# Optimization experiments

Measured on AMD Instinct MI355X. Metric: run time of the kernel, lower is better.

The kernel has to match this reference:

```python
import jax, jax.numpy as jnp
from jax import lax
import numpy as np

B, L, D, F, T, NB = 32, 512, 256, 256, 2048, 256
LN_EPS = 1e-5


def _layer_norm(h, g, b):
    m = jnp.mean(h, axis=-1, keepdims=True)
    v = jnp.mean((h - m) ** 2, axis=-1, keepdims=True)
    return (h - m) * lax.rsqrt(v + LN_EPS) * g + b


def _predictor(h, prm):
    # Conv1d(k=3, pad=1) -> ReLU -> LayerNorm, twice, then Linear(F->1) -> ReLU -> squeeze
    # (dropout is identity in this deterministic reference)
    c1w, c1b, g1, b1, c2w, c2b, g2, b2, lw, lb = prm
    h = lax.conv_general_dilated(h, c1w, (1,), 'SAME', dimension_numbers=('NWC', 'WIO', 'NWC')) + c1b
    h = _layer_norm(jax.nn.relu(h), g1, b1)
    h = lax.conv_general_dilated(h, c2w, (1,), 'SAME', dimension_numbers=('NWC', 'WIO', 'NWC')) + c2b
    h = _layer_norm(jax.nn.relu(h), g2, b2)
    return jax.nn.relu(jnp.einsum('btf,f->bt', h, lw) + lb)  # [B, T]


def _length_regulate(x, dur, t_out):
    # Gather-based equivalent of the dense alignment-matrix matmul in LengthRegulator.LR:
    # frame t maps to phoneme j with cum[j-1] <= t < cum[j]; frames past total duration are zero.
    cum = jnp.cumsum(dur, axis=1)                                          # [B, L]
    t = jnp.arange(t_out)                                                  # [T]
    idx = jax.vmap(lambda c: jnp.searchsorted(c, t, side='right'))(cum)    # [B, T]
    valid = idx < dur.shape[1]
    idx = jnp.clip(idx, 0, dur.shape[1] - 1)
    out = jnp.take_along_axis(x, idx[..., None], axis=1)                   # [B, T, D]
    return jnp.where(valid[..., None], out, jnp.zeros((), x.dtype))


def setup_inputs() -> dict:
    key = jax.random.key(0)
    ks = iter(jax.random.split(key, 64))

    def nrm(shape, s=0.05):
        return jax.random.normal(next(ks), shape, jnp.float32) * s

    inp = dict(
        x=jax.random.normal(next(ks), (B, L, D), jnp.float32),
        d_target=jax.random.randint(next(ks), (B, L), 0, 4, jnp.int32),
        e_target=jax.random.normal(next(ks), (B, T), jnp.float32),
        p_target=jax.random.normal(next(ks), (B, T), jnp.float32),
        mel_max_length=T,
    )
    for p in ('dur', 'en', 'pi'):
        inp[p + '_c1w'] = nrm((3, D, F)); inp[p + '_c1b'] = jnp.zeros((F,), jnp.float32)
        inp[p + '_g1'] = jnp.ones((F,), jnp.float32); inp[p + '_b1'] = jnp.zeros((F,), jnp.float32)
        inp[p + '_c2w'] = nrm((3, F, F)); inp[p + '_c2b'] = jnp.zeros((F,), jnp.float32)
        inp[p + '_g2'] = jnp.ones((F,), jnp.float32); inp[p + '_b2'] = jnp.zeros((F,), jnp.float32)
        inp[p + '_lw'] = nrm((F,)); inp[p + '_lb'] = jnp.zeros((), jnp.float32)
    inp['en_emb'] = nrm((NB, D), 0.1)
    inp['pi_emb'] = nrm((NB, D), 0.1)
    inp['en_bins'] = jnp.linspace(-3.0, 3.0, NB - 1, dtype=jnp.float32)
    inp['pi_bins'] = jnp.linspace(-3.0, 3.0, NB - 1, dtype=jnp.float32)
    return inp


def reference(x, d_target, e_target, p_target, mel_max_length,
              dur_c1w, dur_c1b, dur_g1, dur_b1, dur_c2w, dur_c2b, dur_g2, dur_b2, dur_lw, dur_lb,
              en_c1w, en_c1b, en_g1, en_b1, en_c2w, en_c2b, en_g2, en_b2, en_lw, en_lb,
              pi_c1w, pi_c1b, pi_g1, pi_b1, pi_c2w, pi_c2b, pi_g2, pi_b2, pi_lw, pi_lb,
              en_emb, pi_emb, en_bins, pi_bins):
    dur_prm = (dur_c1w, dur_c1b, dur_g1, dur_b1, dur_c2w, dur_c2b, dur_g2, dur_b2, dur_lw, dur_lb)
    en_prm = (en_c1w, en_c1b, en_g1, en_b1, en_c2w, en_c2b, en_g2, en_b2, en_lw, en_lb)
    pi_prm = (pi_c1w, pi_c1b, pi_g1, pi_b1, pi_c2w, pi_c2b, pi_g2, pi_b2, pi_lw, pi_lb)

    log_dur = _predictor(x, dur_prm)                               # [B, L]
    h = _length_regulate(x, d_target, mel_max_length)              # [B, T, D]

    energy_pred = _predictor(h, en_prm)                            # [B, T]
    e_idx = jnp.searchsorted(en_bins, e_target, side='left')       # torch.bucketize(right=False)
    h = h + jnp.take(en_emb, e_idx, axis=0)

    pitch_pred = _predictor(h, pi_prm)                             # [B, T]
    p_idx = jnp.searchsorted(pi_bins, p_target, side='left')
    h = h + jnp.take(pi_emb, p_idx, axis=0)

    return (h, log_dur, pitch_pred, energy_pred)
```

## Files before the change

kernel.cpp:

```cpp
#include <hip/hip_runtime.h>
#include <hip/hip_bf16.h>
#include <cstddef>

constexpr int B = 32, L = 512, D = 256, F = 256, T = 2048, NB = 256;
constexpr float LN_EPS = 1e-5f;
constexpr int BDIM = 256;
constexpr int WFRAGS = 24 * 16 * 64;

constexpr int N_FH  = 1024;
constexpr int NT_L  = 9;
constexpr int NT_T  = 34;
constexpr int N_DUR = NT_L * B;
constexpr int N_TP  = NT_T * B;

typedef __attribute__((ext_vector_type(8))) short short8;
typedef __attribute__((ext_vector_type(4))) short short4v;
typedef __attribute__((ext_vector_type(4))) float f32x4;

__device__ inline short f2bf(float x) {
    __hip_bfloat16 h = __float2bfloat16(x);
    return __builtin_bit_cast(short, h);
}

__global__ void cumsum_kernel(const int* __restrict__ dt, int* __restrict__ cum) {
    __shared__ int s[L];
    const int b = blockIdx.x, tid = threadIdx.x;
    s[tid] = dt[b * L + tid];
    __syncthreads();
    for (int off = 1; off < L; off <<= 1) {
        int v = (tid >= off) ? s[tid - off] : 0;
        __syncthreads();
        s[tid] += v;
        __syncthreads();
    }
    cum[b * L + tid] = s[tid];
}

__global__ void idx_kernel(const int* __restrict__ cum,
                           const float* __restrict__ et, const float* __restrict__ ebins,
                           const float* __restrict__ pt, const float* __restrict__ pbins,
                           int* __restrict__ gidx, int* __restrict__ eidx, int* __restrict__ pidx) {
    const int r = blockIdx.x * BDIM + threadIdx.x;
    const int b = r >> 11, t = r & (T - 1);
    const int* c = cum + b * L;
    int lo = 0, hi = L;
    while (lo < hi) { const int mid = (lo + hi) >> 1; if (c[mid] <= t) lo = mid + 1; else hi = mid; }
    gidx[r] = (lo < L) ? lo : -1;
    const float e = et[r];
    int el = 0, eh = NB - 1;
    while (el < eh) { const int mid = (el + eh) >> 1; if (ebins[mid] < e) el = mid + 1; else eh = mid; }
    eidx[r] = el;
    const float p = pt[r];
    int pl = 0, ph = NB - 1;
    while (pl < ph) { const int mid = (pl + ph) >> 1; if (pbins[mid] < p) pl = mid + 1; else ph = mid; }
    pidx[r] = pl;
}

__global__ void wprep_kernel(const float* __restrict__ w0, const float* __restrict__ w1,
                             const float* __restrict__ w2, const float* __restrict__ w3,
                             const float* __restrict__ w4, const float* __restrict__ w5,
                             short* __restrict__ wb) {
    const float* ws[6] = {w0, w1, w2, w3, w4, w5};
    const float* w = ws[blockIdx.y];
    short* dst = wb + (size_t)blockIdx.y * WFRAGS * 8;
    const int phi = blockIdx.x * BDIM + threadIdx.x;
    const int kb = phi >> 10;
    const int n16 = (phi >> 6) & 15;
    const int lane = phi & 63;
    const int kconv = kb >> 3, dblk = kb & 7;
    const int kg = lane >> 4;
    const int fcol = (n16 >> 2) * 64 + (lane & 15) * 4 + (n16 & 3);
    const float* src = w + (size_t)kconv * D * F + (dblk * 32 + kg * 8) * F + fcol;
    short8 o;
    #pragma unroll
    for (int j = 0; j < 8; j++) o[j] = f2bf(src[j * F]);
    *(short8*)(dst + (size_t)phi * 8) = o;
}

__global__ void zv_kernel(const float* __restrict__ cb1, const float* __restrict__ g1,
                          const float* __restrict__ b1,
                          const float* __restrict__ w2, const float* __restrict__ cb2,
                          const float* __restrict__ g2, const float* __restrict__ b2,
                          const float* __restrict__ lw, const float* __restrict__ lb,
                          float* __restrict__ zv) {
    __shared__ float z1s[F];
    __shared__ float red[8];
    const int f = threadIdx.x;
    const int wv = f >> 6, lane = f & 63;

    float v = fmaxf(cb1[f], 0.f);
    float s = v, q = v * v;
    #pragma unroll
    for (int msk = 1; msk < 64; msk <<= 1) { s += __shfl_xor(s, msk); q += __shfl_xor(q, msk); }
    if (lane == 0) { red[wv] = s; red[4 + wv] = q; }
    __syncthreads();
    {
        const float S = red[0] + red[1] + red[2] + red[3];
        const float Q = red[4] + red[5] + red[6] + red[7];
        const float m = S * (1.f / 256.f);
        const float var = fmaxf(Q * (1.f / 256.f) - m * m, 0.f);
        const float rs = rsqrtf(var + LN_EPS);
        z1s[f] = (v - m) * rs * g1[f] + b1[f];
    }
    __syncthreads();

    float y = cb2[f];
    for (int d = 0; d < D; d++) {
        y += z1s[d] * (w2[(size_t)d * F + f] + w2[((size_t)D + d) * F + f]
                       + w2[((size_t)2 * D + d) * F + f]);
    }
    v = fmaxf(y, 0.f);
    s = v; q = v * v;
    #pragma unroll
    for (int msk = 1; msk < 64; msk <<= 1) { s += __shfl_xor(s, msk); q += __shfl_xor(q, msk); }
    __syncthreads();
    if (lane == 0) { red[wv] = s; red[4 + wv] = q; }
    __syncthreads();
    const float S = red[0] + red[1] + red[2] + red[3];
    const float Q = red[4] + red[5] + red[6] + red[7];
    const float m = S * (1.f / 256.f);
    const float var = fmaxf(Q * (1.f / 256.f) - m * m, 0.f);
    const float rs = rsqrtf(var + LN_EPS);
    float p = ((v - m) * rs * g2[f] + b2[f]) * lw[f];
    #pragma unroll
    for (int msk = 1; msk < 64; msk <<= 1) p += __shfl_xor(p, msk);
    __syncthreads();
    if (lane == 0) red[wv] = p;
    __syncthreads();
    if (f == 0) zv[0] = fmaxf(red[0] + red[1] + red[2] + red[3] + lb[0], 0.f);
}

__device__ __forceinline__ void conv_mfma16(const short8 (&a)[4], const short8 (&bb)[4],
                                            f32x4 (&acc)[4][4]) {
    __builtin_amdgcn_s_setprio(1);
    #pragma unroll
    for (int m = 0; m < 4; m++)
        #pragma unroll
        for (int n = 0; n < 4; n++)
            acc[m][n] = __builtin_amdgcn_mfma_f32_16x16x32_bf16(a[m], bb[n], acc[m][n], 0, 0, 0);
    __builtin_amdgcn_s_setprio(0);
}

__device__ __forceinline__ void conv_kloop(const short* in_s, const short8* bw,
                                           f32x4 (&acc)[4][4], int w,
                                           int lane, int kg, int lr) {
    const short8* bp = bw + (w * 4) * 64 + lane;
    short8 bA[4], bB[4];
    #pragma unroll
    for (int n = 0; n < 4; n++) bA[n] = bp[n * 64];
    bp += 1024;
    #pragma unroll
    for (int n = 0; n < 4; n++) bB[n] = bp[n * 64];
    bp += 1024;

    #pragma unroll
    for (int kconv = 0; kconv < 3; kconv++) {
        const short* rowp = in_s + (lr + kconv) * 256;
        const int xb = (lr + kconv) & 7;
        #pragma unroll 1
        for (int db = 0; db < 8; db += 2) {
            short8 a[4];
            {
                const short* ab = rowp + (((db * 4 + kg) ^ xb) << 3);
                #pragma unroll
                for (int m = 0; m < 4; m++) a[m] = *(const short8*)(ab + m * 4096);
                conv_mfma16(a, bA, acc);
                #pragma unroll
                for (int n = 0; n < 4; n++) bA[n] = bp[n * 64];
                bp += 1024;
            }
            {
                const short* ab = rowp + ((((db + 1) * 4 + kg) ^ xb) << 3);
                #pragma unroll
                for (int m = 0; m < 4; m++) a[m] = *(const short8*)(ab + m * 4096);
                conv_mfma16(a, bB, acc);
                #pragma unroll
                for (int n = 0; n < 4; n++) bB[n] = bp[n * 64];
                bp += 1024;
            }
        }
    }
}

struct PredParams {
    const short* wb1; const short* wb2;
    const float *cb1, *g1, *b1, *cb2, *g2, *b2, *lw, *lb;
    const int* eidx; const float* emb;
    const float* zv;
    float* out;
    int Tlen;
    int mode;
};

__launch_bounds__(BDIM, 4)
__global__ void mega_kernel(const float* __restrict__ xin,
                            const int* __restrict__ gidx,
                            const int* __restrict__ cum,
                            const int* __restrict__ eidxA,
                            const int* __restrict__ pidxA,
                            const float* __restrict__ eemb,
                            const float* __restrict__ pemb,
                            float* __restrict__ h,
                            PredParams pd, PredParams pe, PredParams pp) {
    __shared__ short in_s[66 * 256];
    __shared__ float red_s[4][64], red_q[4][64];
    __shared__ float row_m[64], row_rs[64];
    __shared__ float dot_p[4][64];

    const int tid = threadIdx.x;
    const int w = tid >> 6, lane = tid & 63;

    int id = blockIdx.x;
    if (id < N_FH) {
        const int row0 = id * 64 + w * 16;
        #pragma unroll 4
        for (int i = 0; i < 16; i++) {
            const int row = row0 + i;
            const int b = row >> 11;
            const int g = gidx[row], ei = eidxA[row], pi = pidxA[row];
            float4 v = make_float4(0.f, 0.f, 0.f, 0.f);
            if (g >= 0) v = *(const float4*)(xin + ((size_t)b * L + g) * D + lane * 4);
            const float4 ev = *(const float4*)(eemb + (size_t)ei * D + lane * 4);
            const float4 pv = *(const float4*)(pemb + (size_t)pi * D + lane * 4);
            v.x += ev.x + pv.x; v.y += ev.y + pv.y; v.z += ev.z + pv.z; v.w += ev.w + pv.w;
            *(float4*)(h + (size_t)row * D + lane * 4) = v;
        }
        return;
    }
    id -= N_FH;

    PredParams P;
    int b, tx;
    if (id < N_DUR) {
        P = pd; b = id / NT_L; tx = id % NT_L;
    } else if (id < N_DUR + N_TP) {
        id -= N_DUR;
        P = pe; b = id / NT_T; tx = id % NT_T;
    } else {
        id -= N_DUR + N_TP;
        P = pp; b = id / NT_T; tx = id % NT_T;
    }
    const int Tlen = P.Tlen;
    const int t0 = tx * 62;
    const int kg = lane >> 4, lr = lane & 15;

    if (P.zv != nullptr) {
        const int ctot = cum[(b + 1) * L - 1];
        if (t0 - 2 >= ctot) {
            if (tid < 62) {
                const int t = t0 + tid;
                if (t < Tlen) P.out[(size_t)b * Tlen + t] = P.zv[0];
            }
            return;
        }
    }

    constexpr int TASKS = 66 * 32;
    constexpr int BATCH = 4;
    const bool has_emb = (P.emb != nullptr);
    for (int base = 0; base < TASKS; base += BATCH * BDIM) {
        float4 fa[BATCH], fb[BATCH], ea[BATCH], eb[BATCH];
        #pragma unroll
        for (int j = 0; j < BATCH; j++) {
            fa[j] = make_float4(0.f, 0.f, 0.f, 0.f); fb[j] = fa[j];
            ea[j] = fa[j]; eb[j] = fa[j];
            const int task = base + j * BDIM + tid;
            if (task < TASKS) {
                const int row = task >> 5, slot = task & 31;
                const int t = t0 - 2 + row;
                if (t >= 0 && t < Tlen) {
                    if (P.mode == 0) {
                        const float* p = xin + ((size_t)b * Tlen + t) * D + slot * 8;
                        fa[j] = *(const float4*)p; fb[j] = *(const float4*)(p + 4);
                    } else {
                        const int g = gidx[b * T + t];
                        if (g >= 0) {
                            const float* p = xin + ((size_t)b * L + g) * D + slot * 8;
                            fa[j] = *(const float4*)p; fb[j] = *(const float4*)(p + 4);
                        }
                        if (has_emb) {
                            const float* er = P.emb + (size_t)P.eidx[b * T + t] * F + slot * 8;
                            ea[j] = *(const float4*)er; eb[j] = *(const float4*)(er + 4);
                        }
                    }
                }
            }
        }
        #pragma unroll
        for (int j = 0; j < BATCH; j++) {
            const int task = base + j * BDIM + tid;
            if (task < TASKS) {
                const int row = task >> 5, slot = task & 31;
                short8 frag;
                frag[0] = f2bf(fa[j].x + ea[j].x); frag[1] = f2bf(fa[j].y + ea[j].y);
                frag[2] = f2bf(fa[j].z + ea[j].z); frag[3] = f2bf(fa[j].w + ea[j].w);
                frag[4] = f2bf(fb[j].x + eb[j].x); frag[5] = f2bf(fb[j].y + eb[j].y);
                frag[6] = f2bf(fb[j].z + eb[j].z); frag[7] = f2bf(fb[j].w + eb[j].w);
                *(short8*)(in_s + row * 256 + ((slot ^ (row & 7)) << 3)) = frag;
            }
        }
    }
    __syncthreads();

    f32x4 acc[4][4];
    #pragma unroll
    for (int m = 0; m < 4; m++)
        #pragma unroll
        for (int n = 0; n < 4; n++)
            acc[m][n] = (f32x4){0.f, 0.f, 0.f, 0.f};
    conv_kloop(in_s, (const short8*)P.wb1, acc, w, lane, kg, lr);

    const int cbase = w * 64 + lr * 4;
    const f32x4 c1v = *(const f32x4*)(P.cb1 + cbase);
    const f32x4 g1v = *(const f32x4*)(P.g1 + cbase);
    const f32x4 b1v = *(const f32x4*)(P.b1 + cbase);

    #pragma unroll
    for (int m = 0; m < 4; m++) {
        #pragma unroll
        for (int reg = 0; reg < 4; reg++) {
            float s = 0.f, q = 0.f;
            #pragma unroll
            for (int n = 0; n < 4; n++) {
                const float v = fmaxf(acc[m][n][reg] + c1v[n], 0.f);
                acc[m][n][reg] = v;
                s += v; q += v * v;
            }
            #pragma unroll
            for (int msk = 1; msk < 16; msk <<= 1) { s += __shfl_xor(s, msk); q += __shfl_xor(q, msk); }
            if (lr == 0) {
                const int r = m * 16 + kg * 4 + reg;
                red_s[w][r] = s; red_q[w][r] = q;
            }
        }
    }
    __syncthreads();
    if (tid < 64) {
        const float s = red_s[0][tid] + red_s[1][tid] + red_s[2][tid] + red_s[3][tid];
        const float q = red_q[0][tid] + red_q[1][tid] + red_q[2][tid] + red_q[3][tid];
        const float mm = s * (1.f / 256.f);
        const float var = fmaxf(q * (1.f / 256.f) - mm * mm, 0.f);
        row_m[tid] = mm;
        row_rs[tid] = rsqrtf(var + LN_EPS);
    }
    if (tid >= 128 && tid < 192) {
        short8 z = {};
        *(short8*)(in_s + 64 * 256 + (tid - 128) * 8) = z;
    }
    __syncthreads();

    #pragma unroll
    for (int m = 0; m < 4; m++) {
        #pragma unroll
        for (int reg = 0; reg < 4; reg++) {
            const int r1 = m * 16 + kg * 4 + reg;
            const int tg = t0 - 1 + r1;
            const bool ok = (tg >= 0) && (tg < Tlen);
            const float mm = row_m[r1], rs = row_rs[r1];
            short4v o;
            #pragma unroll
            for (int n = 0; n < 4; n++) {
                const float v = ok ? (acc[m][n][reg] - mm) * rs * g1v[n] + b1v[n] : 0.f;
                o[n] = f2bf(v);
            }
            *(short4v*)(in_s + r1 * 256 + (((cbase >> 3) ^ (r1 & 7)) << 3) + (cbase & 7)) = o;
        }
    }
    __syncthreads();

    #pragma unroll
    for (int m = 0; m < 4; m++)
        #pragma unroll
        for (int n = 0; n < 4; n++)
            acc[m][n] = (f32x4){0.f, 0.f, 0.f, 0.f};
    conv_kloop(in_s, (const short8*)P.wb2, acc, w, lane, kg, lr);

    const f32x4 c2v = *(const f32x4*)(P.cb2 + cbase);
    const f32x4 g2v = *(const f32x4*)(P.g2 + cbase);
    const f32x4 b2v = *(const f32x4*)(P.b2 + cbase);
    const f32x4 lwv = *(const f32x4*)(P.lw + cbase);

    #pragma unroll
    for (int m = 0; m < 4; m++) {
        #pragma unroll
        for (int reg = 0; reg < 4; reg++) {
            float s = 0.f, q = 0.f;
            #pragma unroll
            for (int n = 0; n < 4; n++) {
                const float v = fmaxf(acc[m][n][reg] + c2v[n], 0.f);
                acc[m][n][reg] = v;
                s += v; q += v * v;
            }
            #pragma unroll
            for (int msk = 1; msk < 16; msk <<= 1) { s += __shfl_xor(s, msk); q += __shfl_xor(q, msk); }
            if (lr == 0) {
                const int r = m * 16 + kg * 4 + reg;
                red_s[w][r] = s; red_q[w][r] = q;
            }
        }
    }
    __syncthreads();
    if (tid < 64) {
        const float s = red_s[0][tid] + red_s[1][tid] + red_s[2][tid] + red_s[3][tid];
        const float q = red_q[0][tid] + red_q[1][tid] + red_q[2][tid] + red_q[3][tid];
        const float mm = s * (1.f / 256.f);
        const float var = fmaxf(q * (1.f / 256.f) - mm * mm, 0.f);
        row_m[tid] = mm;
        row_rs[tid] = rsqrtf(var + LN_EPS);
    }
    __syncthreads();
    #pragma unroll
    for (int m = 0; m < 4; m++) {
        #pragma unroll
        for (int reg = 0; reg < 4; reg++) {
            const int r = m * 16 + kg * 4 + reg;
            const float mm = row_m[r], rs = row_rs[r];
            float p = 0.f;
            #pragma unroll
            for (int n = 0; n < 4; n++)
                p += ((acc[m][n][reg] - mm) * rs * g2v[n] + b2v[n]) * lwv[n];
            #pragma unroll
            for (int msk = 1; msk < 16; msk <<= 1) p += __shfl_xor(p, msk);
            if (lr == 0) dot_p[w][r] = p;
        }
    }
    __syncthreads();
    if (tid < 62) {
        const int t = t0 + tid;
        if (t < Tlen) {
            const float p = dot_p[0][tid] + dot_p[1][tid] + dot_p[2][tid] + dot_p[3][tid] + P.lb[0];
            P.out[(size_t)b * Tlen + t] = fmaxf(p, 0.f);
        }
    }
}

extern "C" void kernel_launch(void* const* d_in, const int* in_sizes, int n_in,
                              void* d_out, int out_size, void* d_ws, size_t ws_size,
                              hipStream_t stream) {
    const float* x        = (const float*)d_in[0];
    const int*   d_target = (const int*)d_in[1];
    const float* e_target = (const float*)d_in[2];
    const float* p_target = (const float*)d_in[3];

    const float* const* P = (const float* const*)d_in;
    const float* en_emb  = (const float*)d_in[35];
    const float* pi_emb  = (const float*)d_in[36];
    const float* en_bins = (const float*)d_in[37];
    const float* pi_bins = (const float*)d_in[38];

    float* out = (float*)d_out;
    float* h        = out;
    float* log_dur  = out + (size_t)B * T * D;
    float* pitch    = log_dur + (size_t)B * L;
    float* energy   = pitch + (size_t)B * T;

    short* wbs  = (short*)d_ws;
    int*   cum  = (int*)(wbs + (size_t)6 * WFRAGS * 8);
    int*   gidx = cum + B * L;
    int*   eidx = gidx + B * T;
    int*   pidx = eidx + B * T;
    float* zvp  = (float*)(pidx + B * T);

    wprep_kernel<<<dim3(WFRAGS / BDIM, 6), BDIM, 0, stream>>>(
        P[5], P[9], P[15], P[19], P[25], P[29], wbs);

    cumsum_kernel<<<B, L, 0, stream>>>(d_target, cum);
    idx_kernel<<<B * T / BDIM, BDIM, 0, stream>>>(
        cum, e_target, en_bins, p_target, pi_bins, gidx, eidx, pidx);

    zv_kernel<<<1, BDIM, 0, stream>>>(
        P[16], P[17], P[18], P[19], P[20], P[21], P[22], P[23], P[24], zvp);

    PredParams dur_p = { wbs + (size_t)0 * WFRAGS * 8, wbs + (size_t)1 * WFRAGS * 8,
                         P[6], P[7], P[8], P[10], P[11], P[12], P[13], P[14],
                         nullptr, nullptr, nullptr, log_dur, L, 0 };
    PredParams en_p  = { wbs + (size_t)2 * WFRAGS * 8, wbs + (size_t)3 * WFRAGS * 8,
                         P[16], P[17], P[18], P[20], P[21], P[22], P[23], P[24],
                         nullptr, nullptr, zvp, energy, T, 1 };
    PredParams pi_p  = { wbs + (size_t)4 * WFRAGS * 8, wbs + (size_t)5 * WFRAGS * 8,
                         P[26], P[27], P[28], P[30], P[31], P[32], P[33], P[34],
                         eidx, en_emb, nullptr, pitch, T, 1 };

    mega_kernel<<<N_FH + N_DUR + 2 * N_TP, BDIM, 0, stream>>>(
        x, gidx, cum, eidx, pidx, en_emb, pi_emb, h, dur_p, en_p, pi_p);
}
```

Before: 153.1 us.

## Merge preprocessing kernels into one preamble launch and reorder mega-kernel blocks

Replaces four small launches (weight prep, cumsum, index search, zero-vector predictor) with a single preamble kernel whose blocks pick their role from the block index. The cumsum and the binary searches now share one block per batch, so the cumulative durations are read from shared memory. The mega kernel now schedules predictor blocks first and the memory-bound frame-gather blocks last, so heavy work starts earlier and the gather fills the tail. This cuts launch overhead and inter-kernel gaps, but the idx work now runs on only 32 blocks instead of 256.

```diff
diff --git a/kernel.cpp b/kernel.cpp
--- a/kernel.cpp
+++ b/kernel.cpp
@@ -12,6 +12,11 @@
 constexpr int NT_T  = 34;
 constexpr int N_DUR = NT_L * B;
 constexpr int N_TP  = NT_T * B;
+constexpr int N_PRED = N_DUR + 2 * N_TP;
+
+constexpr int PRE_WPREP = 576;
+constexpr int PRE_IDX   = 32;
+constexpr int PRE_TOTAL = PRE_WPREP + PRE_IDX + 1;
 
 typedef __attribute__((ext_vector_type(8))) short short8;
 typedef __attribute__((ext_vector_type(4))) short short4v;
@@ -22,112 +27,123 @@
     return __builtin_bit_cast(short, h);
 }
 
-__global__ void cumsum_kernel(const int* __restrict__ dt, int* __restrict__ cum) {
-    __shared__ int s[L];
-    const int b = blockIdx.x, tid = threadIdx.x;
-    s[tid] = dt[b * L + tid];
-    __syncthreads();
-    for (int off = 1; off < L; off <<= 1) {
-        int v = (tid >= off) ? s[tid - off] : 0;
-        __syncthreads();
-        s[tid] += v;
-        __syncthreads();
-    }
-    cum[b * L + tid] = s[tid];
-}
-
-__global__ void idx_kernel(const int* __restrict__ cum,
-                           const float* __restrict__ et, const float* __restrict__ ebins,
-                           const float* __restrict__ pt, const float* __restrict__ pbins,
-                           int* __restrict__ gidx, int* __restrict__ eidx, int* __restrict__ pidx) {
-    const int r = blockIdx.x * BDIM + threadIdx.x;
-    const int b = r >> 11, t = r & (T - 1);
-    const int* c = cum + b * L;
-    int lo = 0, hi = L;
-    while (lo < hi) { const int mid = (lo + hi) >> 1; if (c[mid] <= t) lo = mid + 1; else hi = mid; }
-    gidx[r] = (lo < L) ? lo : -1;
-    const float e = et[r];
-    int el = 0, eh = NB - 1;
-    while (el < eh) { const int mid = (el + eh) >> 1; if (ebins[mid] < e) el = mid + 1; else eh = mid; }
-    eidx[r] = el;
-    const float p = pt[r];
-    int pl = 0, ph = NB - 1;
-    while (pl < ph) { const int mid = (pl + ph) >> 1; if (pbins[mid] < p) pl = mid + 1; else ph = mid; }
-    pidx[r] = pl;
-}
-
-__global__ void wprep_kernel(const float* __restrict__ w0, const float* __restrict__ w1,
-                             const float* __restrict__ w2, const float* __restrict__ w3,
-                             const float* __restrict__ w4, const float* __restrict__ w5,
-                             short* __restrict__ wb) {
-    const float* ws[6] = {w0, w1, w2, w3, w4, w5};
-    const float* w = ws[blockIdx.y];
-    short* dst = wb + (size_t)blockIdx.y * WFRAGS * 8;
-    const int phi = blockIdx.x * BDIM + threadIdx.x;
-    const int kb = phi >> 10;
-    const int n16 = (phi >> 6) & 15;
-    const int lane = phi & 63;
-    const int kconv = kb >> 3, dblk = kb & 7;
-    const int kg = lane >> 4;
-    const int fcol = (n16 >> 2) * 64 + (lane & 15) * 4 + (n16 & 3);
-    const float* src = w + (size_t)kconv * D * F + (dblk * 32 + kg * 8) * F + fcol;
-    short8 o;
-    #pragma unroll
-    for (int j = 0; j < 8; j++) o[j] = f2bf(src[j * F]);
-    *(short8*)(dst + (size_t)phi * 8) = o;
-}
-
-__global__ void zv_kernel(const float* __restrict__ cb1, const float* __restrict__ g1,
-                          const float* __restrict__ b1,
-                          const float* __restrict__ w2, const float* __restrict__ cb2,
-                          const float* __restrict__ g2, const float* __restrict__ b2,
-                          const float* __restrict__ lw, const float* __restrict__ lb,
-                          float* __restrict__ zv) {
-    __shared__ float z1s[F];
+__global__ void preamble_kernel(const float* __restrict__ w0, const float* __restrict__ w1,
+                                const float* __restrict__ w2, const float* __restrict__ w3,
+                                const float* __restrict__ w4, const float* __restrict__ w5,
+                                const int* __restrict__ dt,
+                                const float* __restrict__ et, const float* __restrict__ ebins,
+                                const float* __restrict__ pt, const float* __restrict__ pbins,
+                                const float* __restrict__ zcb1, const float* __restrict__ zg1,
+                                const float* __restrict__ zb1, const float* __restrict__ zw2,
+                                const float* __restrict__ zcb2, const float* __restrict__ zg2,
+                                const float* __restrict__ zb2, const float* __restrict__ zlw,
+                                const float* __restrict__ zlb,
+                                short* __restrict__ wb, int* __restrict__ cum,
+                                int* __restrict__ gidx, int* __restrict__ eidx,
+                                int* __restrict__ pidx, float* __restrict__ zv) {
+    __shared__ int   cs[512];
+    __shared__ float z1s[256];
     __shared__ float red[8];
-    const int f = threadIdx.x;
-    const int wv = f >> 6, lane = f & 63;
-
-    float v = fmaxf(cb1[f], 0.f);
-    float s = v, q = v * v;
-    #pragma unroll
-    for (int msk = 1; msk < 64; msk <<= 1) { s += __shfl_xor(s, msk); q += __shfl_xor(q, msk); }
-    if (lane == 0) { red[wv] = s; red[4 + wv] = q; }
-    __syncthreads();
+
+    const int tid = threadIdx.x;
+    int id = blockIdx.x;
+
+    if (id < PRE_WPREP) {
+        const float* ws[6] = {w0, w1, w2, w3, w4, w5};
+        const float* w = ws[id / 96];
+        short* dst = wb + (size_t)(id / 96) * WFRAGS * 8;
+        const int phi = (id % 96) * BDIM + tid;
+        const int kb = phi >> 10;
+        const int n16 = (phi >> 6) & 15;
+        const int lane = phi & 63;
+        const int kconv = kb >> 3, dblk = kb & 7;
+        const int kg = lane >> 4;
+        const int fcol = (n16 >> 2) * 64 + (lane & 15) * 4 + (n16 & 3);
+        const float* src = w + (size_t)kconv * D * F + (dblk * 32 + kg * 8) * F + fcol;
+        short8 o;
+        #pragma unroll
+        for (int j = 0; j < 8; j++) o[j] = f2bf(src[j * F]);
+        *(short8*)(dst + (size_t)phi * 8) = o;
+        return;
+    }
+    id -= PRE_WPREP;
+
+    if (id < PRE_IDX) {
+        const int b = id;
+        cs[tid] = dt[b * L + tid];
+        cs[tid + 256] = dt[b * L + tid + 256];
+        __syncthreads();
+        for (int off = 1; off < 512; off <<= 1) {
+            const int v0 = (tid >= off) ? cs[tid - off] : 0;
+            const int v1 = (tid + 256 >= off) ? cs[tid + 256 - off] : 0;
+            __syncthreads();
+            cs[tid] += v0; cs[tid + 256] += v1;
+            __syncthreads();
+        }
+        cum[b * L + tid] = cs[tid];
+        cum[b * L + tid + 256] = cs[tid + 256];
+        #pragma unroll
+        for (int i = 0; i < 8; i++) {
+            const int t = tid + i * 256;
+            const int r = b * T + t;
+            int lo = 0, hi = L;
+            while (lo < hi) { const int mid = (lo + hi) >> 1; if (cs[mid] <= t) lo = mid + 1; else hi = mid; }
+            gidx[r] = (lo < L) ? lo : -1;
+            const float e = et[r];
+            int el = 0, eh = NB - 1;
+            while (el < eh) { const int mid = (el + eh) >> 1; if (ebins[mid] < e) el = mid + 1; else eh = mid; }
+            eidx[r] = el;
+            const float p = pt[r];
+            int pl = 0, ph = NB - 1;
+            while (pl < ph) { const int mid = (pl + ph) >> 1; if (pbins[mid] < p) pl = mid + 1; else ph = mid; }
+            pidx[r] = pl;
+        }
+        return;
+    }
+
     {
+        const int f = tid;
+        const int wv = f >> 6, lane = f & 63;
+        float v = fmaxf(zcb1[f], 0.f);
+        float s = v, q = v * v;
+        #pragma unroll
+        for (int msk = 1; msk < 64; msk <<= 1) { s += __shfl_xor(s, msk); q += __shfl_xor(q, msk); }
+        if (lane == 0) { red[wv] = s; red[4 + wv] = q; }
+        __syncthreads();
+        {
+            const float S = red[0] + red[1] + red[2] + red[3];
+            const float Q = red[4] + red[5] + red[6] + red[7];
+            const float m = S * (1.f / 256.f);
+            const float var = fmaxf(Q * (1.f / 256.f) - m * m, 0.f);
+            const float rs = rsqrtf(var + LN_EPS);
+            z1s[f] = (v - m) * rs * zg1[f] + zb1[f];
+        }
+        __syncthreads();
+        float y = zcb2[f];
+        for (int d = 0; d < D; d++) {
+            y += z1s[d] * (zw2[(size_t)d * F + f] + zw2[((size_t)D + d) * F + f]
+                           + zw2[((size_t)2 * D + d) * F + f]);
+        }
+        v = fmaxf(y, 0.f);
+        s = v; q = v * v;
+        #pragma unroll
+        for (int msk = 1; msk < 64; msk <<= 1) { s += __shfl_xor(s, msk); q += __shfl_xor(q, msk); }
+        __syncthreads();
+        if (lane == 0) { red[wv] = s; red[4 + wv] = q; }
+        __syncthreads();
         const float S = red[0] + red[1] + red[2] + red[3];
         const float Q = red[4] + red[5] + red[6] + red[7];
         const float m = S * (1.f / 256.f);
         const float var = fmaxf(Q * (1.f / 256.f) - m * m, 0.f);
         const float rs = rsqrtf(var + LN_EPS);
-        z1s[f] = (v - m) * rs * g1[f] + b1[f];
-    }
-    __syncthreads();
-
-    float y = cb2[f];
-    for (int d = 0; d < D; d++) {
-        y += z1s[d] * (w2[(size_t)d * F + f] + w2[((size_t)D + d) * F + f]
-                       + w2[((size_t)2 * D + d) * F + f]);
-    }
-    v = fmaxf(y, 0.f);
-    s = v; q = v * v;
-    #pragma unroll
-    for (int msk = 1; msk < 64; msk <<= 1) { s += __shfl_xor(s, msk); q += __shfl_xor(q, msk); }
-    __syncthreads();
-    if (lane == 0) { red[wv] = s; red[4 + wv] = q; }
-    __syncthreads();
-    const float S = red[0] + red[1] + red[2] + red[3];
-    const float Q = red[4] + red[5] + red[6] + red[7];
-    const float m = S * (1.f / 256.f);
-    const float var = fmaxf(Q * (1.f / 256.f) - m * m, 0.f);
-    const float rs = rsqrtf(var + LN_EPS);
-    float p = ((v - m) * rs * g2[f] + b2[f]) * lw[f];
-    #pragma unroll
-    for (int msk = 1; msk < 64; msk <<= 1) p += __shfl_xor(p, msk);
-    __syncthreads();
-    if (lane == 0) red[wv] = p;
-    __syncthreads();
-    if (f == 0) zv[0] = fmaxf(red[0] + red[1] + red[2] + red[3] + lb[0], 0.f);
+        float p = ((v - m) * rs * zg2[f] + zb2[f]) * zlw[f];
+        #pragma unroll
+        for (int msk = 1; msk < 64; msk <<= 1) p += __shfl_xor(p, msk);
+        __syncthreads();
+        if (lane == 0) red[wv] = p;
+        __syncthreads();
+        if (f == 0) zv[0] = fmaxf(red[0] + red[1] + red[2] + red[3] + zlb[0], 0.f);
+    }
 }
 
 __device__ __forceinline__ void conv_mfma16(const short8 (&a)[4], const short8 (&bb)[4],
@@ -211,8 +227,9 @@
     const int w = tid >> 6, lane = tid & 63;
 
     int id = blockIdx.x;
-    if (id < N_FH) {
-        const int row0 = id * 64 + w * 16;
+    if (id >= N_PRED) {
+        const int fid = id - N_PRED;
+        const int row0 = fid * 64 + w * 16;
         #pragma unroll 4
         for (int i = 0; i < 16; i++) {
             const int row = row0 + i;
@@ -227,7 +244,6 @@
         }
         return;
     }
-    id -= N_FH;
 
     PredParams P;
     int b, tx;
@@ -461,15 +477,11 @@
     int*   pidx = eidx + B * T;
     float* zvp  = (float*)(pidx + B * T);
 
-    wprep_kernel<<<dim3(WFRAGS / BDIM, 6), BDIM, 0, stream>>>(
-        P[5], P[9], P[15], P[19], P[25], P[29], wbs);
-
-    cumsum_kernel<<<B, L, 0, stream>>>(d_target, cum);
-    idx_kernel<<<B * T / BDIM, BDIM, 0, stream>>>(
-        cum, e_target, en_bins, p_target, pi_bins, gidx, eidx, pidx);
-
-    zv_kernel<<<1, BDIM, 0, stream>>>(
-        P[16], P[17], P[18], P[19], P[20], P[21], P[22], P[23], P[24], zvp);
+    preamble_kernel<<<PRE_TOTAL, BDIM, 0, stream>>>(
+        P[5], P[9], P[15], P[19], P[25], P[29],
+        d_target, e_target, en_bins, p_target, pi_bins,
+        P[16], P[17], P[18], P[19], P[20], P[21], P[22], P[23], P[24],
+        wbs, cum, gidx, eidx, pidx, zvp);
 
     PredParams dur_p = { wbs + (size_t)0 * WFRAGS * 8, wbs + (size_t)1 * WFRAGS * 8,
                          P[6], P[7], P[8], P[10], P[11], P[12], P[13], P[14],
@@ -481,6 +493,6 @@
                          P[26], P[27], P[28], P[30], P[31], P[32], P[33], P[34],
                          eidx, en_emb, nullptr, pitch, T, 1 };
 
-    mega_kernel<<<N_FH + N_DUR + 2 * N_TP, BDIM, 0, stream>>>(
+    mega_kernel<<<N_PRED + N_FH, BDIM, 0, stream>>>(
         x, gidx, cum, eidx, pidx, en_emb, pi_emb, h, dur_p, en_p, pi_p);
 }
```

Measured after the change: 138.7 us (median of 2 runs). 9.4% less time.
